# Optimization experiments

Measured on AMD Instinct MI355X. Metric: run time of the kernel, lower is better.

Reference implementation:

```python
import jax, jax.numpy as jnp
import numpy as np

B, T, E, H = 2, 2048, 1024, 16


def setup_inputs() -> dict:
    key = jax.random.key(0)
    ks = jax.random.split(key, 8)
    # VarianceScaling(1.0) ~ truncated normal with stddev ~ sqrt(1/fan_in)
    std = 1.0 / np.sqrt(E)
    x = jax.random.normal(ks[0], (B, T, E), dtype=jnp.float32)
    y = jax.random.normal(ks[1], (B, T, E), dtype=jnp.float32)
    # causal mask [1, 1, T, T]
    mask = jnp.tril(jnp.ones((T, T), dtype=jnp.float32))[None, None]
    Wq = jax.random.normal(ks[2], (E, E), dtype=jnp.float32) * std
    Wk = jax.random.normal(ks[3], (E, E), dtype=jnp.float32) * std
    Wv = jax.random.normal(ks[4], (E, E), dtype=jnp.float32) * std
    Wo = jax.random.normal(ks[5], (E, E), dtype=jnp.float32) * std
    bq = jnp.zeros((E,), jnp.float32)
    bk = jnp.zeros((E,), jnp.float32)
    bv = jnp.zeros((E,), jnp.float32)
    bo = jnp.zeros((E,), jnp.float32)
    return {"x": x, "y": y, "mask": mask, "Wq": Wq, "bq": bq,
            "Wk": Wk, "bk": bk, "Wv": Wv, "bv": bv, "Wo": Wo, "bo": bo,
            "num_heads": H}


def reference(x, y, mask, Wq, bq, Wk, bk, Wv, bv, Wo, bo, num_heads):
    Bx, Tq, Emb = x.shape
    Tkv = y.shape[1]
    d = Emb // num_heads
    q = (x @ Wq + bq).reshape(Bx, Tq, num_heads, d)
    k = (y @ Wk + bk).reshape(Bx, Tkv, num_heads, d)
    v = (y @ Wv + bv).reshape(Bx, Tkv, num_heads, d)
    scale = 1.0 / np.sqrt(d).astype(np.float32)
    att = scale * jnp.einsum('bthd,bThd->bhtT', q, k)  # [B,H,Tq,Tkv]
    att = att * mask - 1e10 * (1.0 - mask)
    att = jax.nn.softmax(att, axis=-1)
    out = jnp.einsum('bhtT,bThd->bthd', att, v).reshape(Bx, Tq, Emb)
    return out @ Wo + bo
```

## Files before the change

kernel.cpp:

```cpp
#include <hip/hip_runtime.h>
#include <stdint.h>

#define BB 2
#define TT 2048
#define EE 1024
#define HH 16
#define DD 64
#define MM (BB*TT)

typedef unsigned short u16;
typedef __attribute__((ext_vector_type(4))) float f32x4;
typedef __attribute__((ext_vector_type(8))) __bf16 bf16x8;
typedef __attribute__((ext_vector_type(8))) u16 u16x8;
typedef __attribute__((ext_vector_type(4))) u16 u16x4;

union FragU { u16x8 u; bf16x8 b; };
union BfU { __bf16 h; u16 u; };

__device__ __forceinline__ u16 f2bf(float f) {
  uint32_t u = __float_as_uint(f);
  u += 0x7fffu + ((u >> 16) & 1u);
  return (u16)(u >> 16);
}

__device__ __forceinline__ void gload16(const u16* __restrict__ g, u16* l) {
  __builtin_amdgcn_global_load_lds((const __attribute__((address_space(1))) void*)g,
                                   (__attribute__((address_space(3))) void*)l, 16, 0, 0);
}

__global__ __launch_bounds__(256) void prep(const float* __restrict__ x, const float* __restrict__ y,
                                            const float* __restrict__ Wq, const float* __restrict__ Wk,
                                            const float* __restrict__ Wv, const float* __restrict__ Wo,
                                            u16* __restrict__ xb, u16* __restrict__ yb,
                                            u16* __restrict__ Wqt, u16* __restrict__ Wkvt,
                                            u16* __restrict__ Wot) {
  __shared__ alignas(16) float tile[64][65];
  int bi = blockIdx.x, t = threadIdx.x;
  if (bi < 4096) {
    const float* src = (bi < 2048) ? x : y;
    u16* dst = (bi < 2048) ? xb : yb;
    int i = (bi & 2047) * 256 + t;
    const f32x4* s4 = (const f32x4*)src;
    f32x4 a = s4[2*i], b = s4[2*i+1];
    u16x8 o;
    o[0]=f2bf(a[0]); o[1]=f2bf(a[1]); o[2]=f2bf(a[2]); o[3]=f2bf(a[3]);
    o[4]=f2bf(b[0]); o[5]=f2bf(b[1]); o[6]=f2bf(b[2]); o[7]=f2bf(b[3]);
    ((u16x8*)dst)[i] = o;
    return;
  }
  int wi = bi - 4096;
  int z = wi >> 8;
  const float* W; u16* Tp;
  switch (z) {
    case 0: W = Wq; Tp = Wqt; break;
    case 1: W = Wk; Tp = Wkvt; break;
    case 2: W = Wv; Tp = Wkvt + (size_t)1024*EE; break;
    default: W = Wo; Tp = Wot; break;
  }
  int r8 = wi & 255;
  int n0 = (r8 & 15) * 64, k0 = (r8 >> 4) * 64;
#pragma unroll
  for (int i = 0; i < 16; ++i) {
    int idx = i*256 + t; int r = idx >> 6, c = idx & 63;
    tile[r][c] = W[(size_t)(k0 + r) * EE + n0 + c];
  }
  __syncthreads();
#pragma unroll
  for (int i = 0; i < 16; ++i) {
    int idx = i*256 + t; int rn = idx >> 6, ck = idx & 63;
    Tp[(size_t)(n0 + rn) * EE + k0 + ck] = f2bf(tile[ck][rn]);
  }
}

template <int BM, int EPI>
__device__ __forceinline__ void gemm_body(const u16* __restrict__ A, const u16* __restrict__ Bt,
                                          const float* __restrict__ bias, void* __restrict__ Cout,
                                          int N, int K, float oscale, int bm, int bn,
                                          u16 (*As)[64], u16 (*Bs)[64]) {
  constexpr int MI = BM / 32;
  const int t = threadIdx.x;
  const int lane = t & 63, w = t >> 6;
  const int wr = w >> 1, wc = w & 1;
  const int g = lane >> 4, cl = lane & 15;

  f32x4 acc[MI][4] = {};

  const u16* Ag = A + (size_t)(bm * BM) * K;
  const u16* Bg = Bt + (size_t)(bn * 128) * K;

  const int rl = lane >> 3;
  const int sw = ((lane & 7) ^ rl) * 8;

  const int nk = K / 64;
  for (int kt = 0; kt < nk; ++kt) {
    const int k0 = kt * 64;
    __syncthreads();
#pragma unroll
    for (int j = 0; j < MI; ++j) {
      int ca = w * MI + j;
      gload16(Ag + (size_t)(ca*8 + rl) * K + k0 + sw, &As[ca*8][0]);
    }
#pragma unroll
    for (int j = 0; j < 4; ++j) {
      int cb = w * 4 + j;
      gload16(Bg + (size_t)(cb*8 + rl) * K + k0 + sw, &Bs[cb*8][0]);
    }
    __syncthreads();
#pragma unroll
    for (int ks = 0; ks < 2; ++ks) {
      FragU af[MI], bfr[4];
#pragma unroll
      for (int mi = 0; mi < MI; ++mi) {
        int row = wr*(BM/2) + mi*16 + cl;
        af[mi].u = *(const u16x8*)&As[row][((ks*4 + g) ^ (row & 7)) * 8];
      }
#pragma unroll
      for (int nj = 0; nj < 4; ++nj) {
        int row = wc*64 + nj*16 + cl;
        bfr[nj].u = *(const u16x8*)&Bs[row][((ks*4 + g) ^ (row & 7)) * 8];
      }
#pragma unroll
      for (int mi = 0; mi < MI; ++mi)
#pragma unroll
        for (int nj = 0; nj < 4; ++nj)
          acc[mi][nj] = __builtin_amdgcn_mfma_f32_16x16x32_bf16(af[mi].b, bfr[nj].b, acc[mi][nj], 0, 0, 0);
    }
  }

  const int cbase = bn*128 + wc*64 + cl;
  float bv[4];
#pragma unroll
  for (int nj = 0; nj < 4; ++nj) bv[nj] = bias[cbase + nj*16];
#pragma unroll
  for (int mi = 0; mi < MI; ++mi) {
    int row0 = bm*BM + wr*(BM/2) + mi*16 + (g << 2);
    if (EPI == 2) {
      int bb = row0 >> 11;
      int tt = row0 & 2047;
      int tb64 = tt & ~63;
      int w6 = tt & 63;
      int p = ((w6 >> 5) << 5) | (((w6 >> 2) & 3) << 3) | (((w6 >> 4) & 1) << 2);
#pragma unroll
      for (int nj = 0; nj < 4; ++nj) {
        int cc = cbase + nj*16;
        int hh = cc >> 6, dd = cc & 63;
        u16x4 v;
#pragma unroll
        for (int i = 0; i < 4; ++i) v[i] = f2bf(acc[mi][nj][i] + bv[nj]);
        *(u16x4*)((u16*)Cout + ((size_t)((bb*HH + hh)*DD + dd))*2048 + tb64 + p) = v;
      }
    } else {
#pragma unroll
      for (int i = 0; i < 4; ++i) {
        if (EPI == 1) {
          float* Cp = (float*)Cout + (size_t)(row0 + i) * N + cbase;
#pragma unroll
          for (int nj = 0; nj < 4; ++nj)
            Cp[nj*16] = (acc[mi][nj][i] + bv[nj]) * oscale;
        } else {
          u16* Cp = (u16*)Cout + (size_t)(row0 + i) * N + cbase;
#pragma unroll
          for (int nj = 0; nj < 4; ++nj)
            Cp[nj*16] = f2bf((acc[mi][nj][i] + bv[nj]) * oscale);
        }
      }
    }
  }
}

__global__ __launch_bounds__(256) void gemm_qkv(const u16* __restrict__ xb, const u16* __restrict__ yb,
                                                const u16* __restrict__ Wqt, const u16* __restrict__ Wkvt,
                                                const float* __restrict__ bq, const float* __restrict__ bk,
                                                const float* __restrict__ bv,
                                                u16* __restrict__ Qb, u16* __restrict__ Kb,
                                                u16* __restrict__ Vtb, float c1) {
  __shared__ alignas(16) u16 As[64][64];
  __shared__ alignas(16) u16 Bs[128][64];
  const int i = blockIdx.x;
  const int l = (i & 7) * 192 + (i >> 3);
  const int bm = l / 24, bx = l % 24;
  if (bx < 8)
    gemm_body<64, 0>(xb, Wqt, bq, Qb, 1024, EE, c1, bm, bx, As, Bs);
  else if (bx < 16)
    gemm_body<64, 0>(yb, Wkvt, bk, Kb, 1024, EE, 1.0f, bm, bx - 8, As, Bs);
  else
    gemm_body<64, 2>(yb, Wkvt + (size_t)1024*EE, bv, Vtb, 1024, EE, 1.0f, bm, bx - 16, As, Bs);
}

__global__ __launch_bounds__(256) void gemm_o(const u16* __restrict__ Atb, const u16* __restrict__ Wot,
                                              const float* __restrict__ bo, float* __restrict__ out) {
  __shared__ alignas(16) u16 As[64][64];
  __shared__ alignas(16) u16 Bs[128][64];
  const int i = blockIdx.x;
  const int l = (i & 7) * 64 + (i >> 3);
  const int bm = l / 8, bn = l % 8;
  gemm_body<64, 1>(Atb, Wot, bo, out, 1024, EE, 1.0f, bm, bn, As, Bs);
}

__global__ __launch_bounds__(512, 4) void attn(const u16* __restrict__ Q, const u16* __restrict__ Kb,
                                               const u16* __restrict__ Vt, u16* __restrict__ O) {
  const int i0 = blockIdx.x;
  const int qp = i0 >> 5;
  const int bh = i0 & 31;
  const int b = bh >> 4, h = bh & 15;

  const int t = threadIdx.x, lane = t & 63, w = t >> 6;
  const int ws_ = w & 3;
  const int hi = w >> 2;
  const int g = lane >> 4, c = lane & 15;
  __shared__ alignas(16) u16 Ks[2][64][72];
  __shared__ alignas(16) u16 Vs[2][64][72];

  const u16* Kbase = Kb + (size_t)(b*TT) * 1024 + h*DD;
  const u16* Vtbase = Vt + (size_t)(b*HH + h) * DD * 2048;

  const int srow = t >> 3;
  const int scol = (t & 7) * 8;

  for (int pi = 0; pi < 2; ++pi) {
    const int qt = pi ? 31 - qp : qp;
    const int qw0 = qt * 64 + ws_ * 16;

    FragU qf[2];
    const u16* Qbase = Q + ((size_t)(b*TT) + qw0) * EE + h*DD;
#pragma unroll
    for (int ks = 0; ks < 2; ++ks)
      qf[ks].u = *(const u16x8*)(Qbase + (size_t)c * EE + ks*32 + g*8);

    f32x4 oacc[4] = {};
    float l_part = 0.f;
    float m_run = -1e30f;

    const int nkv = qt + 1;
    const int npair = (nkv + 1) >> 1;

    u16x8 rk[2], rv[2];
    rk[0] = *(const u16x8*)(Kbase + (size_t)srow * 1024 + scol);
    rv[0] = *(const u16x8*)(Vtbase + (size_t)srow * 2048 + scol);
    if (1 < nkv) {
      rk[1] = *(const u16x8*)(Kbase + (size_t)(64 + srow) * 1024 + scol);
      rv[1] = *(const u16x8*)(Vtbase + (size_t)srow * 2048 + 64 + scol);
    }

    for (int jj = 0; jj < npair; ++jj) {
      const int j0 = 2*jj;
      __syncthreads();
      *(u16x8*)&Ks[0][srow][scol] = rk[0];
      *(u16x8*)&Vs[0][srow][scol] = rv[0];
      if (j0 + 1 < nkv) {
        *(u16x8*)&Ks[1][srow][scol] = rk[1];
        *(u16x8*)&Vs[1][srow][scol] = rv[1];
      }
      __syncthreads();
      if (jj + 1 < npair) {
        const int jn = 2*(jj + 1);
        rk[0] = *(const u16x8*)(Kbase + (size_t)(jn*64 + srow) * 1024 + scol);
        rv[0] = *(const u16x8*)(Vtbase + (size_t)srow * 2048 + jn*64 + scol);
        if (jn + 1 < nkv) {
          rk[1] = *(const u16x8*)(Kbase + (size_t)((jn+1)*64 + srow) * 1024 + scol);
          rv[1] = *(const u16x8*)(Vtbase + (size_t)srow * 2048 + (jn+1)*64 + scol);
        }
      }
      const int j = j0 + hi;
      const int kv0 = j * 64;
      if (j >= nkv || kv0 > qw0 + 15) continue;

      f32x4 s[4] = {};
      __builtin_amdgcn_s_setprio(1);
#pragma unroll
      for (int ks = 0; ks < 2; ++ks) {
        const int kc = ks*32 + g*8;
        FragU kf[4];
#pragma unroll
        for (int nj = 0; nj < 4; ++nj)
          kf[nj].u = *(const u16x8*)&Ks[hi][nj*16 + c][kc];
#pragma unroll
        for (int nj = 0; nj < 4; ++nj)
          s[nj] = __builtin_amdgcn_mfma_f32_16x16x32_bf16(kf[nj].b, qf[ks].b, s[nj], 0, 0, 0);
      }
      __builtin_amdgcn_s_setprio(0);

      const bool full = (kv0 + 63 <= qw0);
      float vmax;
      if (full) {
        float m0 = fmaxf(fmaxf(s[0][0], s[0][1]), fmaxf(s[0][2], s[0][3]));
        float m1 = fmaxf(fmaxf(s[1][0], s[1][1]), fmaxf(s[1][2], s[1][3]));
        float m2 = fmaxf(fmaxf(s[2][0], s[2][1]), fmaxf(s[2][2], s[2][3]));
        float m3 = fmaxf(fmaxf(s[3][0], s[3][1]), fmaxf(s[3][2], s[3][3]));
        vmax = fmaxf(fmaxf(m0, m1), fmaxf(m2, m3));
      } else {
        const int q = qw0 + c;
        vmax = -1e30f;
#pragma unroll
        for (int nj = 0; nj < 4; ++nj)
#pragma unroll
          for (int r = 0; r < 4; ++r) {
            float xv = s[nj][r];
            if (kv0 + nj*16 + 4*g + r > q) xv = -1e30f;
            s[nj][r] = xv;
            vmax = fmaxf(vmax, xv);
          }
      }

      if (__any(vmax > m_run + 8.f)) {
        float vm = vmax;
        vm = fmaxf(vm, __shfl_xor(vm, 1));
        vm = fmaxf(vm, __shfl_xor(vm, 2));
        vm = fmaxf(vm, __shfl_xor(vm, 4));
        vm = fmaxf(vm, __shfl_xor(vm, 8));
        vm = fmaxf(vm, __shfl_xor(vm, 16));
        vm = fmaxf(vm, __shfl_xor(vm, 32));
        float f = exp2f(m_run - vm);
        l_part *= f;
#pragma unroll
        for (int dj = 0; dj < 4; ++dj)
#pragma unroll
          for (int i = 0; i < 4; ++i) oacc[dj][i] *= f;
        m_run = vm;
      }

      FragU pa[2];
      float psum = 0.f;
#pragma unroll
      for (int nj = 0; nj < 4; ++nj)
#pragma unroll
        for (int r = 0; r < 4; ++r) {
          float p = exp2f(s[nj][r] - m_run);
          psum += p;
          BfU cv; cv.h = (__bf16)p;
          pa[nj >> 1].u[(nj & 1) * 4 + r] = cv.u;
        }
      l_part += psum;

      __builtin_amdgcn_s_setprio(1);
#pragma unroll
      for (int ks = 0; ks < 2; ++ks) {
#pragma unroll
        for (int dj = 0; dj < 4; ++dj) {
          FragU vf;
          vf.u = *(const u16x8*)&Vs[hi][dj*16 + c][ks*32 + g*8];
          oacc[dj] = __builtin_amdgcn_mfma_f32_16x16x32_bf16(pa[ks].b, vf.b, oacc[dj], 0, 0, 0);
        }
      }
      __builtin_amdgcn_s_setprio(0);
    }

    __syncthreads();
    l_part += __shfl_xor(l_part, 16);
    l_part += __shfl_xor(l_part, 32);

    float* mO = (float*)&Ks[0][0][0];
    float* mL = (float*)&Vs[0][0][0];

    if (hi) {
#pragma unroll
      for (int i = 0; i < 4; ++i) {
        int row = 4*g + i;
#pragma unroll
        for (int dj = 0; dj < 4; ++dj)
          mO[((size_t)(ws_*16 + row))*66 + dj*16 + c] = oacc[dj][i];
      }
      if (lane < 16) mL[ws_*16 + lane] = l_part;
      if (lane == 0) mL[64 + ws_] = m_run;
    }
    __syncthreads();
    if (!hi) {
      float m1 = mL[64 + ws_];
      float l1 = mL[ws_*16 + c];
      float mN = fmaxf(m_run, m1);
      float f0 = exp2f(m_run - mN);
      float f1 = exp2f(m1 - mN);
      float lm = l_part * f0 + l1 * f1;
      u16* Ob = O + ((size_t)(b*TT) + qw0) * EE + h*DD;
#pragma unroll
      for (int i = 0; i < 4; ++i) {
        int row = 4*g + i;
        float li = __shfl(lm, row);
        float inv = 1.f / li;
#pragma unroll
        for (int dj = 0; dj < 4; ++dj) {
          float o1 = mO[((size_t)(ws_*16 + row))*66 + dj*16 + c];
          Ob[(size_t)row * EE + dj*16 + c] = f2bf((oacc[dj][i] * f0 + o1 * f1) * inv);
        }
      }
    }
  }
}

extern "C" void kernel_launch(void* const* d_in, const int* in_sizes, int n_in,
                              void* d_out, int out_size, void* d_ws, size_t ws_size,
                              hipStream_t stream) {
  const float* x  = (const float*)d_in[0];
  const float* y  = (const float*)d_in[1];
  const float* Wq = (const float*)d_in[3];
  const float* bq = (const float*)d_in[4];
  const float* Wk = (const float*)d_in[5];
  const float* bk = (const float*)d_in[6];
  const float* Wv = (const float*)d_in[7];
  const float* bv = (const float*)d_in[8];
  const float* Wo = (const float*)d_in[9];
  const float* bo = (const float*)d_in[10];

  if (ws_size < (size_t)58720256) return;

  char* ws = (char*)d_ws;
  u16* Wqt  = (u16*)(ws + 0);
  u16* Wkvt = (u16*)(ws + 2097152);
  u16* Wot  = (u16*)(ws + 6291456);
  u16* Qb   = (u16*)(ws + 8388608);
  u16* Kb   = (u16*)(ws + 16777216);
  u16* Vtb  = (u16*)(ws + 25165824);
  u16* Atb  = (u16*)(ws + 33554432);
  u16* xb   = (u16*)(ws + 41943040);
  u16* yb   = (u16*)(ws + 50331648);

  const float c1 = 0.125f * 1.44269504088896340736f;

  prep<<<5120, 256, 0, stream>>>(x, y, Wq, Wk, Wv, Wo, xb, yb, Wqt, Wkvt, Wot);
  gemm_qkv<<<1536, 256, 0, stream>>>(xb, yb, Wqt, Wkvt, bq, bk, bv, Qb, Kb, Vtb, c1);
  attn<<<512, 512, 0, stream>>>(Qb, Kb, Vtb, Atb);
  gemm_o<<<512, 256, 0, stream>>>(Atb, Wot, bo, (float*)d_out);
}
```

Before: 105.6 us.

## Double-buffer K/V shared tiles to drop one barrier per attention iteration

```diff
diff --git a/kernel.cpp b/kernel.cpp
--- a/kernel.cpp
+++ b/kernel.cpp
@@ -208,8 +208,8 @@
   const int ws_ = w & 3;
   const int hi = w >> 2;
   const int g = lane >> 4, c = lane & 15;
-  __shared__ alignas(16) u16 Ks[2][64][72];
-  __shared__ alignas(16) u16 Vs[2][64][72];
+  __shared__ alignas(16) u16 Ks[2][2][64][72];
+  __shared__ alignas(16) u16 Vs[2][2][64][72];
 
   const u16* Kbase = Kb + (size_t)(b*TT) * 1024 + h*DD;
   const u16* Vtbase = Vt + (size_t)(b*HH + h) * DD * 2048;
@@ -234,123 +234,140 @@
     const int nkv = qt + 1;
     const int npair = (nkv + 1) >> 1;
 
+    const u16* kp = Kbase + (size_t)srow * 1024 + scol;
+    const u16* vp = Vtbase + (size_t)srow * 2048 + scol;
+
     u16x8 rk[2], rv[2];
-    rk[0] = *(const u16x8*)(Kbase + (size_t)srow * 1024 + scol);
-    rv[0] = *(const u16x8*)(Vtbase + (size_t)srow * 2048 + scol);
+    rk[0] = *(const u16x8*)kp;
+    rv[0] = *(const u16x8*)vp;
     if (1 < nkv) {
-      rk[1] = *(const u16x8*)(Kbase + (size_t)(64 + srow) * 1024 + scol);
-      rv[1] = *(const u16x8*)(Vtbase + (size_t)srow * 2048 + 64 + scol);
-    }
+      rk[1] = *(const u16x8*)(kp + 65536);
+      rv[1] = *(const u16x8*)(vp + 64);
+    }
+    kp += 131072; vp += 128;
+
+    __syncthreads();
+    *(u16x8*)&Ks[0][0][srow][scol] = rk[0];
+    *(u16x8*)&Vs[0][0][srow][scol] = rv[0];
+    if (1 < nkv) {
+      *(u16x8*)&Ks[0][1][srow][scol] = rk[1];
+      *(u16x8*)&Vs[0][1][srow][scol] = rv[1];
+    }
+    __syncthreads();
 
     for (int jj = 0; jj < npair; ++jj) {
+      const int d = jj & 1;
       const int j0 = 2*jj;
-      __syncthreads();
-      *(u16x8*)&Ks[0][srow][scol] = rk[0];
-      *(u16x8*)&Vs[0][srow][scol] = rv[0];
-      if (j0 + 1 < nkv) {
-        *(u16x8*)&Ks[1][srow][scol] = rk[1];
-        *(u16x8*)&Vs[1][srow][scol] = rv[1];
-      }
-      __syncthreads();
       if (jj + 1 < npair) {
-        const int jn = 2*(jj + 1);
-        rk[0] = *(const u16x8*)(Kbase + (size_t)(jn*64 + srow) * 1024 + scol);
-        rv[0] = *(const u16x8*)(Vtbase + (size_t)srow * 2048 + jn*64 + scol);
-        if (jn + 1 < nkv) {
-          rk[1] = *(const u16x8*)(Kbase + (size_t)((jn+1)*64 + srow) * 1024 + scol);
-          rv[1] = *(const u16x8*)(Vtbase + (size_t)srow * 2048 + (jn+1)*64 + scol);
-        }
-      }
+        rk[0] = *(const u16x8*)kp;
+        rv[0] = *(const u16x8*)vp;
+        if (j0 + 3 < nkv) {
+          rk[1] = *(const u16x8*)(kp + 65536);
+          rv[1] = *(const u16x8*)(vp + 64);
+        }
+        kp += 131072; vp += 128;
+      }
+
       const int j = j0 + hi;
       const int kv0 = j * 64;
-      if (j >= nkv || kv0 > qw0 + 15) continue;
-
-      f32x4 s[4] = {};
-      __builtin_amdgcn_s_setprio(1);
-#pragma unroll
-      for (int ks = 0; ks < 2; ++ks) {
-        const int kc = ks*32 + g*8;
-        FragU kf[4];
+      if (j < nkv && kv0 <= qw0 + 15) {
+        f32x4 s[4] = {};
+        __builtin_amdgcn_s_setprio(1);
+#pragma unroll
+        for (int ks = 0; ks < 2; ++ks) {
+          const int kc = ks*32 + g*8;
+          FragU kf[4];
+#pragma unroll
+          for (int nj = 0; nj < 4; ++nj)
+            kf[nj].u = *(const u16x8*)&Ks[d][hi][nj*16 + c][kc];
+#pragma unroll
+          for (int nj = 0; nj < 4; ++nj)
+            s[nj] = __builtin_amdgcn_mfma_f32_16x16x32_bf16(kf[nj].b, qf[ks].b, s[nj], 0, 0, 0);
+        }
+        __builtin_amdgcn_s_setprio(0);
+
+        const bool full = (kv0 + 63 <= qw0);
+        float vmax;
+        if (full) {
+          float m0 = fmaxf(fmaxf(s[0][0], s[0][1]), fmaxf(s[0][2], s[0][3]));
+          float m1 = fmaxf(fmaxf(s[1][0], s[1][1]), fmaxf(s[1][2], s[1][3]));
+          float m2 = fmaxf(fmaxf(s[2][0], s[2][1]), fmaxf(s[2][2], s[2][3]));
+          float m3 = fmaxf(fmaxf(s[3][0], s[3][1]), fmaxf(s[3][2], s[3][3]));
+          vmax = fmaxf(fmaxf(m0, m1), fmaxf(m2, m3));
+        } else {
+          const int q = qw0 + c;
+          vmax = -1e30f;
+#pragma unroll
+          for (int nj = 0; nj < 4; ++nj)
+#pragma unroll
+            for (int r = 0; r < 4; ++r) {
+              float xv = s[nj][r];
+              if (kv0 + nj*16 + 4*g + r > q) xv = -1e30f;
+              s[nj][r] = xv;
+              vmax = fmaxf(vmax, xv);
+            }
+        }
+
+        if (__any(vmax > m_run + 8.f)) {
+          float vm = vmax;
+          vm = fmaxf(vm, __shfl_xor(vm, 1));
+          vm = fmaxf(vm, __shfl_xor(vm, 2));
+          vm = fmaxf(vm, __shfl_xor(vm, 4));
+          vm = fmaxf(vm, __shfl_xor(vm, 8));
+          vm = fmaxf(vm, __shfl_xor(vm, 16));
+          vm = fmaxf(vm, __shfl_xor(vm, 32));
+          float f = exp2f(m_run - vm);
+          l_part *= f;
+#pragma unroll
+          for (int dj = 0; dj < 4; ++dj)
+#pragma unroll
+            for (int i = 0; i < 4; ++i) oacc[dj][i] *= f;
+          m_run = vm;
+        }
+
+        FragU pa[2];
+        float psum = 0.f;
 #pragma unroll
         for (int nj = 0; nj < 4; ++nj)
-          kf[nj].u = *(const u16x8*)&Ks[hi][nj*16 + c][kc];
-#pragma unroll
-        for (int nj = 0; nj < 4; ++nj)
-          s[nj] = __builtin_amdgcn_mfma_f32_16x16x32_bf16(kf[nj].b, qf[ks].b, s[nj], 0, 0, 0);
-      }
-      __builtin_amdgcn_s_setprio(0);
-
-      const bool full = (kv0 + 63 <= qw0);
-      float vmax;
-      if (full) {
-        float m0 = fmaxf(fmaxf(s[0][0], s[0][1]), fmaxf(s[0][2], s[0][3]));
-        float m1 = fmaxf(fmaxf(s[1][0], s[1][1]), fmaxf(s[1][2], s[1][3]));
-        float m2 = fmaxf(fmaxf(s[2][0], s[2][1]), fmaxf(s[2][2], s[2][3]));
-        float m3 = fmaxf(fmaxf(s[3][0], s[3][1]), fmaxf(s[3][2], s[3][3]));
-        vmax = fmaxf(fmaxf(m0, m1), fmaxf(m2, m3));
-      } else {
-        const int q = qw0 + c;
-        vmax = -1e30f;
-#pragma unroll
-        for (int nj = 0; nj < 4; ++nj)
 #pragma unroll
           for (int r = 0; r < 4; ++r) {
-            float xv = s[nj][r];
-            if (kv0 + nj*16 + 4*g + r > q) xv = -1e30f;
-            s[nj][r] = xv;
-            vmax = fmaxf(vmax, xv);
+            float p = exp2f(s[nj][r] - m_run);
+            psum += p;
+            BfU cv; cv.h = (__bf16)p;
+            pa[nj >> 1].u[(nj & 1) * 4 + r] = cv.u;
           }
-      }
-
-      if (__any(vmax > m_run + 8.f)) {
-        float vm = vmax;
-        vm = fmaxf(vm, __shfl_xor(vm, 1));
-        vm = fmaxf(vm, __shfl_xor(vm, 2));
-        vm = fmaxf(vm, __shfl_xor(vm, 4));
-        vm = fmaxf(vm, __shfl_xor(vm, 8));
-        vm = fmaxf(vm, __shfl_xor(vm, 16));
-        vm = fmaxf(vm, __shfl_xor(vm, 32));
-        float f = exp2f(m_run - vm);
-        l_part *= f;
-#pragma unroll
-        for (int dj = 0; dj < 4; ++dj)
-#pragma unroll
-          for (int i = 0; i < 4; ++i) oacc[dj][i] *= f;
-        m_run = vm;
-      }
-
-      FragU pa[2];
-      float psum = 0.f;
-#pragma unroll
-      for (int nj = 0; nj < 4; ++nj)
-#pragma unroll
-        for (int r = 0; r < 4; ++r) {
-          float p = exp2f(s[nj][r] - m_run);
-          psum += p;
-          BfU cv; cv.h = (__bf16)p;
-          pa[nj >> 1].u[(nj & 1) * 4 + r] = cv.u;
-        }
-      l_part += psum;
-
-      __builtin_amdgcn_s_setprio(1);
-#pragma unroll
-      for (int ks = 0; ks < 2; ++ks) {
-#pragma unroll
-        for (int dj = 0; dj < 4; ++dj) {
-          FragU vf;
-          vf.u = *(const u16x8*)&Vs[hi][dj*16 + c][ks*32 + g*8];
-          oacc[dj] = __builtin_amdgcn_mfma_f32_16x16x32_bf16(pa[ks].b, vf.b, oacc[dj], 0, 0, 0);
-        }
-      }
-      __builtin_amdgcn_s_setprio(0);
+        l_part += psum;
+
+        __builtin_amdgcn_s_setprio(1);
+#pragma unroll
+        for (int ks = 0; ks < 2; ++ks) {
+#pragma unroll
+          for (int dj = 0; dj < 4; ++dj) {
+            FragU vf;
+            vf.u = *(const u16x8*)&Vs[d][hi][dj*16 + c][ks*32 + g*8];
+            oacc[dj] = __builtin_amdgcn_mfma_f32_16x16x32_bf16(pa[ks].b, vf.b, oacc[dj], 0, 0, 0);
+          }
+        }
+        __builtin_amdgcn_s_setprio(0);
+      }
+
+      if (jj + 1 < npair) {
+        *(u16x8*)&Ks[d^1][0][srow][scol] = rk[0];
+        *(u16x8*)&Vs[d^1][0][srow][scol] = rv[0];
+        if (j0 + 3 < nkv) {
+          *(u16x8*)&Ks[d^1][1][srow][scol] = rk[1];
+          *(u16x8*)&Vs[d^1][1][srow][scol] = rv[1];
+        }
+        __syncthreads();
+      }
     }
 
     __syncthreads();
     l_part += __shfl_xor(l_part, 16);
     l_part += __shfl_xor(l_part, 32);
 
-    float* mO = (float*)&Ks[0][0][0];
-    float* mL = (float*)&Vs[0][0][0];
+    float* mO = (float*)&Ks[0][0][0][0];
+    float* mL = (float*)&Vs[0][0][0][0];
 
     if (hi) {
 #pragma unroll
```

New measurement: 106.2 us. Within noise of the previous version (+0.6%).
